# Kernel tuning notes

Hardware: AMD Instinct MI355X
Metric: run time of the kernel (lower is better)

## Reference

```python
import jax, jax.numpy as jnp
import numpy as np

NEG_INF = -1e30

def setup_inputs() -> dict:
    key = jax.random.key(0)
    kC, kQ, kw = jax.random.split(key, 3)
    B, D, Lc, Lq = 32, 128, 2048, 64
    C = jax.random.normal(kC, (B, D, Lc), dtype=jnp.float32)
    Q = jax.random.normal(kQ, (B, D, Lq), dtype=jnp.float32)
    qmask = jnp.ones((B, Lq), dtype=jnp.float32)
    # trilinear weight, uniform(-sqrt(1/D), sqrt(1/D)) as in the torch init
    lim = (1.0 / D) ** 0.5
    w = jax.random.uniform(kw, (3 * D,), dtype=jnp.float32, minval=-lim, maxval=lim)
    return {"C": C, "Q": Q, "qmask": qmask, "w": w}

def reference(C, Q, qmask, w):
    # C: (B, D, Lc), Q: (B, D, Lq), qmask: (B, Lq), w: (3D,)
    Ct = jnp.transpose(C, (0, 2, 1))  # (B, Lc, D)
    Qt = jnp.transpose(Q, (0, 2, 1))  # (B, Lq, D)
    D = Ct.shape[-1]
    w1, w2, w3 = w[:D], w[D:2 * D], w[2 * D:]
    # trilinear similarity S[b,i,j] = Ct[b,i].w1 + Qt[b,j].w2 + (Ct[b,i]*Qt[b,j]).w3
    # computed WITHOUT the (B,Lc,Lq,3D) intermediate
    sc = Ct @ w1                                   # (B, Lc)
    sq = Qt @ w2                                   # (B, Lq)
    scq = jnp.einsum('bid,bjd->bij', Ct * w3, Qt)  # (B, Lc, Lq)
    S = sc[:, :, None] + sq[None if False else slice(None), None, :] + scq  # (B, Lc, Lq)
    m = qmask[:, None, :]                          # (B, 1, Lq)
    S1 = jax.nn.softmax(S * m + (1.0 - m) * NEG_INF, axis=2)  # over query axis
    S2 = jax.nn.softmax(S, axis=1)                             # over context axis
    A = jnp.einsum('bij,bjd->bid', S1, Qt)                     # (B, Lc, D)
    S1S2T = jnp.einsum('bij,bkj->bik', S1, S2)                 # (B, Lc, Lc) via S1 @ S2^T
    Bm = jnp.einsum('bik,bkd->bid', S1S2T, Ct)                 # (B, Lc, D)
    out = jnp.concatenate([Ct, A, Ct * A, Ct * Bm], axis=2)    # (B, Lc, 4D)
    # dropout is identity in eval mode
    return jnp.transpose(out, (0, 2, 1))                       # (B, 4D, Lc)
```

## Files before the change

### kernel.cpp

```cpp
#include <hip/hip_runtime.h>

#define LC 2048
#define DD 128
#define LQ 64
#define NPART 16
#define PAD 136

typedef unsigned short u16;
typedef unsigned int u32;
typedef __attribute__((ext_vector_type(8))) short bf16x8;
typedef __attribute__((ext_vector_type(4))) float f32x4;

__device__ inline u16 f2b(float f) {
  u32 u = __float_as_uint(f);
  u32 r = (u + 0x7fffu + ((u >> 16) & 1u)) >> 16;
  return (u16)r;
}
__device__ inline float b2f(u16 u) { return __uint_as_float(((u32)u) << 16); }
__device__ inline u32 pack2(float a, float b) {
  return (u32)f2b(a) | ((u32)f2b(b) << 16);
}

__global__ __launch_bounds__(64) void k0_sq(const float* __restrict__ Q,
                                            const float* __restrict__ w,
                                            float* __restrict__ sqg) {
  int b = blockIdx.x, j = threadIdx.x;
  const float* Qb = Q + (size_t)b * DD * LQ + j;
  float acc = 0.f;
#pragma unroll 16
  for (int d = 0; d < DD; ++d) acc = fmaf(Qb[d * LQ], w[DD + d], acc);
  sqg[b * LQ + j] = acc;
}

__global__ __launch_bounds__(256) void k13(const float* __restrict__ C,
                                           const float* __restrict__ Q,
                                           const float* __restrict__ w,
                                           const float* __restrict__ sqg,
                                           u16* __restrict__ Eg,
                                           float* __restrict__ Tu_part,
                                           float* __restrict__ Z_part, int B) {
  __shared__ u16 ldsA[128 * PAD];
  __shared__ u16 ldsB[64 * PAD];
  __shared__ float scL[128];
  __shared__ float sqs[64];
  int b = blockIdx.y, bx = blockIdx.x;
  int i0 = bx * 128, t = threadIdx.x;
  const float* Cb = C + (size_t)b * DD * LC;
  const float* Qb = Q + (size_t)b * DD * LQ;
  if (t < 64) sqs[t] = sqg[b * LQ + t];
  int i_st = t & 127, dh = t >> 7;
  float scp = 0.f;
  {
    const float* Cp = Cb + (size_t)dh * 64 * LC + i0 + i_st;
#pragma unroll
    for (int dp = 0; dp < 32; ++dp) {
      int d = dh * 64 + 2 * dp;
      float c0 = Cp[(size_t)(2 * dp) * LC];
      float c1 = Cp[(size_t)(2 * dp + 1) * LC];
      scp = fmaf(c0, w[d], fmaf(c1, w[d + 1], scp));
      *(u32*)&ldsA[i_st * PAD + d] = pack2(c0, c1);
    }
    if (dh == 0) scL[i_st] = scp;
  }
  {
    int j = t & 63, dg = t >> 6;
    const float* Qp = Qb + j;
#pragma unroll
    for (int dp = 0; dp < 16; ++dp) {
      int d = dg * 32 + 2 * dp;
      float q0 = Qp[(size_t)d * LQ] * w[2 * DD + d];
      float q1 = Qp[(size_t)(d + 1) * LQ] * w[2 * DD + d + 1];
      *(u32*)&ldsB[j * PAD + d] = pack2(q0, q1);
    }
  }
  __syncthreads();
  if (dh == 1) scL[i_st] += scp;
  int lane = t & 63, wv = t >> 6;
  int lr = lane & 15, kg = lane >> 4;
  f32x4 acc[2][4];
#pragma unroll
  for (int mt = 0; mt < 2; ++mt)
#pragma unroll
    for (int nt = 0; nt < 4; ++nt) acc[mt][nt] = (f32x4){0.f, 0.f, 0.f, 0.f};
#pragma unroll
  for (int ks = 0; ks < 4; ++ks) {
    bf16x8 af[2], bf[4];
#pragma unroll
    for (int mt = 0; mt < 2; ++mt)
      af[mt] = *(bf16x8*)&ldsA[((wv * 2 + mt) * 16 + lr) * PAD + ks * 32 + kg * 8];
#pragma unroll
    for (int nt = 0; nt < 4; ++nt)
      bf[nt] = *(bf16x8*)&ldsB[(nt * 16 + lr) * PAD + ks * 32 + kg * 8];
#pragma unroll
    for (int mt = 0; mt < 2; ++mt)
#pragma unroll
      for (int nt = 0; nt < 4; ++nt)
        acc[mt][nt] = __builtin_amdgcn_mfma_f32_16x16x32_bf16(af[mt], bf[nt],
                                                              acc[mt][nt], 0, 0, 0);
  }
  __syncthreads();
#pragma unroll
  for (int mt = 0; mt < 2; ++mt) {
    int ib = (wv * 2 + mt) * 16 + kg * 4;
#pragma unroll
    for (int nt = 0; nt < 4; ++nt) {
      int j = nt * 16 + lr;
      float sqv = sqs[j];
      float e0 = __expf(acc[mt][nt][0] + scL[ib + 0] + sqv);
      float e1 = __expf(acc[mt][nt][1] + scL[ib + 1] + sqv);
      float e2 = __expf(acc[mt][nt][2] + scL[ib + 2] + sqv);
      float e3 = __expf(acc[mt][nt][3] + scL[ib + 3] + sqv);
      u32 pk[2] = {pack2(e0, e1), pack2(e2, e3)};
      *(uint2*)&ldsB[j * PAD + ib] = *(uint2*)pk;
    }
  }
  {
    int d = t >> 1, half = t & 1;
    const float* src = Cb + (size_t)d * LC + i0 + half * 64;
#pragma unroll
    for (int ip = 0; ip < 16; ++ip) {
      float4 v = *(const float4*)&src[ip * 4];
      u32 pk[2] = {pack2(v.x, v.y), pack2(v.z, v.w)};
      *(uint2*)&ldsA[d * PAD + half * 64 + ip * 4] = *(uint2*)pk;
    }
  }
  __syncthreads();
  if (t < 64) {
    const u32* row = (const u32*)&ldsB[t * PAD];
    float z = 0.f;
#pragma unroll
    for (int q = 0; q < 64; ++q) {
      u32 v = row[q];
      z += b2f((u16)v) + b2f((u16)(v >> 16));
    }
    Z_part[((size_t)bx * B + b) * LQ + t] = z;
  }
  {
    int i = t >> 1, half = t & 1;
    u32 opk[16];
#pragma unroll
    for (int q = 0; q < 16; ++q) {
      u16 a0 = ldsB[(half * 32 + 2 * q) * PAD + i];
      u16 a1 = ldsB[(half * 32 + 2 * q + 1) * PAD + i];
      opk[q] = (u32)a0 | ((u32)a1 << 16);
    }
    u16* dst = Eg + ((size_t)b * LC + i0 + i) * LQ + half * 32;
#pragma unroll
    for (int q = 0; q < 4; ++q) *(uint4*)&dst[q * 8] = *(uint4*)&opk[q * 4];
  }
  f32x4 tacc[2][4];
#pragma unroll
  for (int mt = 0; mt < 2; ++mt)
#pragma unroll
    for (int nt = 0; nt < 4; ++nt) tacc[mt][nt] = (f32x4){0.f, 0.f, 0.f, 0.f};
#pragma unroll
  for (int ks = 0; ks < 4; ++ks) {
    bf16x8 af[2], bf[4];
#pragma unroll
    for (int mt = 0; mt < 2; ++mt)
      af[mt] = *(bf16x8*)&ldsA[((wv * 2 + mt) * 16 + lr) * PAD + ks * 32 + kg * 8];
#pragma unroll
    for (int nt = 0; nt < 4; ++nt)
      bf[nt] = *(bf16x8*)&ldsB[(nt * 16 + lr) * PAD + ks * 32 + kg * 8];
#pragma unroll
    for (int mt = 0; mt < 2; ++mt)
#pragma unroll
      for (int nt = 0; nt < 4; ++nt)
        tacc[mt][nt] = __builtin_amdgcn_mfma_f32_16x16x32_bf16(af[mt], bf[nt],
                                                               tacc[mt][nt], 0, 0, 0);
  }
  float* Tp = Tu_part + ((size_t)bx * B + b) * LQ * DD;
#pragma unroll
  for (int mt = 0; mt < 2; ++mt)
#pragma unroll
    for (int nt = 0; nt < 4; ++nt) {
      int j = nt * 16 + lr;
      int db = (wv * 2 + mt) * 16 + kg * 4;
      *(f32x4*)&Tp[(size_t)j * DD + db] = tacc[mt][nt];
    }
}

__global__ __launch_bounds__(256) void k3b(const float* __restrict__ Tu_part,
                                           const float* __restrict__ Z_part,
                                           u16* __restrict__ TzT, int B) {
  __shared__ float Tsm[16][68];
  __shared__ float ziL[64];
  int b = blockIdx.y, d0 = blockIdx.x * 16;
  int t = threadIdx.x;
  int dd = t & 15, jg = t >> 4;
  float acc[4] = {};
#pragma unroll
  for (int p = 0; p < NPART; ++p) {
    const float* src = Tu_part + ((size_t)p * B + b) * LQ * DD + d0 + dd;
#pragma unroll
    for (int jj = 0; jj < 4; ++jj) acc[jj] += src[(jg * 4 + jj) * DD];
  }
  if (t < 64) {
    float z = 0.f;
#pragma unroll
    for (int p = 0; p < NPART; ++p) z += Z_part[((size_t)p * B + b) * LQ + t];
    ziL[t] = 1.f / z;
  }
  *(float4*)&Tsm[dd][jg * 4] = make_float4(acc[0], acc[1], acc[2], acc[3]);
  __syncthreads();
  if (t < 128) {
    int d = t >> 3, seg = t & 7;
    u32 pk[4];
#pragma unroll
    for (int q = 0; q < 4; ++q) {
      int j = seg * 8 + q * 2;
      pk[q] = pack2(Tsm[d][j] * ziL[j], Tsm[d][j + 1] * ziL[j + 1]);
    }
    *(uint4*)&TzT[((size_t)b * DD + d0 + d) * LQ + seg * 8] = *(uint4*)pk;
  }
}

__global__ __launch_bounds__(256) void k4(const u16* __restrict__ Eg,
                                          const float* __restrict__ qmask,
                                          const float* __restrict__ Q,
                                          const u16* __restrict__ TzT,
                                          const float* __restrict__ C,
                                          float* __restrict__ out) {
  __shared__ u16 S1L[128 * 72];
  __shared__ u16 QtL[128 * 72];
  __shared__ u16 TzL[128 * 72];
  __shared__ float mkL[64];
  int b = blockIdx.y, i0 = blockIdx.x * 128, t = threadIdx.x;
  if (t < 64) mkL[t] = qmask[b * LQ + t];
  __syncthreads();
  {
    int row = t >> 1, half = t & 1;
    const float* qsrc = Q + (size_t)b * DD * LQ + row * LQ + half * 32;
    u32 qpk[16];
#pragma unroll
    for (int q = 0; q < 16; ++q) qpk[q] = pack2(qsrc[2 * q], qsrc[2 * q + 1]);
#pragma unroll
    for (int q = 0; q < 4; ++q)
      *(uint4*)&QtL[row * 72 + half * 32 + q * 8] = *(uint4*)&qpk[q * 4];
    const u16* tsrc = TzT + ((size_t)b * DD + row) * LQ + half * 32;
#pragma unroll
    for (int q = 0; q < 4; ++q)
      *(uint4*)&TzL[row * 72 + half * 32 + q * 8] = *(const uint4*)&tsrc[q * 8];
    const u16* esrc = Eg + ((size_t)b * LC + i0 + row) * LQ + half * 32;
    u16 lv[32];
#pragma unroll
    for (int q = 0; q < 4; ++q)
      *(uint4*)&lv[q * 8] = *(const uint4*)&esrc[q * 8];
    float ev[32], ps = 0.f;
#pragma unroll
    for (int q = 0; q < 32; ++q) {
      ev[q] = b2f(lv[q]) * mkL[half * 32 + q];
      ps += ev[q];
    }
    ps += __shfl_xor(ps, 1);
    float inv = 1.f / fmaxf(ps, 1e-30f);
    u32 opk[16];
#pragma unroll
    for (int q = 0; q < 16; ++q)
      opk[q] = pack2(ev[2 * q] * inv, ev[2 * q + 1] * inv);
#pragma unroll
    for (int q = 0; q < 4; ++q)
      *(uint4*)&S1L[row * 72 + half * 32 + q * 8] = *(uint4*)&opk[q * 4];
  }
  __syncthreads();
  int lane = t & 63, wv = t >> 6;
  int lr = lane & 15, kg = lane >> 4;
  bf16x8 Bf[2][2];
#pragma unroll
  for (int it = 0; it < 2; ++it)
#pragma unroll
    for (int ks = 0; ks < 2; ++ks)
      Bf[it][ks] =
          *(bf16x8*)&S1L[(wv * 32 + it * 16 + lr) * 72 + ks * 32 + kg * 8];
  const float* Cb = C + (size_t)b * DD * LC + i0;
  float* outb = out + (size_t)b * 4 * DD * LC + i0;
#pragma unroll
  for (int dt = 0; dt < 8; ++dt) {
    bf16x8 QA[2], TA[2];
#pragma unroll
    for (int ks = 0; ks < 2; ++ks) {
      QA[ks] = *(bf16x8*)&QtL[(dt * 16 + lr) * 72 + ks * 32 + kg * 8];
      TA[ks] = *(bf16x8*)&TzL[(dt * 16 + lr) * 72 + ks * 32 + kg * 8];
    }
#pragma unroll
    for (int it = 0; it < 2; ++it) {
      f32x4 accA = {0.f, 0.f, 0.f, 0.f}, accB = {0.f, 0.f, 0.f, 0.f};
      accA = __builtin_amdgcn_mfma_f32_16x16x32_bf16(QA[0], Bf[it][0], accA, 0, 0, 0);
      accA = __builtin_amdgcn_mfma_f32_16x16x32_bf16(QA[1], Bf[it][1], accA, 0, 0, 0);
      accB = __builtin_amdgcn_mfma_f32_16x16x32_bf16(TA[0], Bf[it][0], accB, 0, 0, 0);
      accB = __builtin_amdgcn_mfma_f32_16x16x32_bf16(TA[1], Bf[it][1], accB, 0, 0, 0);
      int ii = wv * 32 + it * 16 + lr;
#pragma unroll
      for (int r = 0; r < 4; ++r) {
        int d = dt * 16 + kg * 4 + r;
        float c = Cb[(size_t)d * LC + ii];
        float a = accA[r], bm = accB[r];
        outb[(size_t)d * LC + ii] = c;
        outb[(size_t)(DD + d) * LC + ii] = a;
        outb[(size_t)(2 * DD + d) * LC + ii] = c * a;
        outb[(size_t)(3 * DD + d) * LC + ii] = c * bm;
      }
    }
  }
}

extern "C" void kernel_launch(void* const* d_in, const int* in_sizes, int n_in,
                              void* d_out, int out_size, void* d_ws, size_t ws_size,
                              hipStream_t stream) {
  const float* C = (const float*)d_in[0];
  const float* Q = (const float*)d_in[1];
  const float* qmask = (const float*)d_in[2];
  const float* w = (const float*)d_in[3];
  float* out = (float*)d_out;
  int B = in_sizes[2] / LQ;

  char* p = (char*)d_ws;
  u16* Eg = (u16*)p;            p += (size_t)B * LC * LQ * 2;
  u16* TzT = (u16*)p;           p += (size_t)B * DD * LQ * 2;
  float* Tu_part = (float*)p;   p += (size_t)NPART * B * LQ * DD * 4;
  float* Z_part = (float*)p;    p += (size_t)NPART * B * LQ * 4;
  float* sqg = (float*)p;

  k0_sq<<<B, 64, 0, stream>>>(Q, w, sqg);
  k13<<<dim3(NPART, B), 256, 0, stream>>>(C, Q, w, sqg, Eg, Tu_part, Z_part, B);
  k3b<<<dim3(DD / 16, B), 256, 0, stream>>>(Tu_part, Z_part, TzT, B);
  k4<<<dim3(LC / 128, B), 256, 0, stream>>>(Eg, qmask, Q, TzT, C, out);
}
```

Measured before the change: 76.91 us.

## Fuse sq and row-softmax normalization into k13, drop k0 and k4 LDS staging

Removes the separate k0_sq launch by computing the query-weight dot product inside k13 while Q is staged. The masked row softmax for S1 is finished in k13 using cross-lane shuffle reductions, so normalized S1 is written to global memory instead of raw exponentials. k4 then loads its MFMA operands straight from global memory (S1, Q converted to bf16 in registers, TzT) instead of staging them through shared memory, which removes its LDS buffers and barriers. In exchange, k13 does extra shuffle and normalization work, and k4 relies on uncoalesced global fragment loads that may be repeated across waves.

```diff
diff --git a/kernel.cpp b/kernel.cpp
--- a/kernel.cpp
+++ b/kernel.cpp
@@ -21,33 +21,23 @@
   return (u32)f2b(a) | ((u32)f2b(b) << 16);
 }
 
-__global__ __launch_bounds__(64) void k0_sq(const float* __restrict__ Q,
-                                            const float* __restrict__ w,
-                                            float* __restrict__ sqg) {
-  int b = blockIdx.x, j = threadIdx.x;
-  const float* Qb = Q + (size_t)b * DD * LQ + j;
-  float acc = 0.f;
-#pragma unroll 16
-  for (int d = 0; d < DD; ++d) acc = fmaf(Qb[d * LQ], w[DD + d], acc);
-  sqg[b * LQ + j] = acc;
-}
-
 __global__ __launch_bounds__(256) void k13(const float* __restrict__ C,
                                            const float* __restrict__ Q,
                                            const float* __restrict__ w,
-                                           const float* __restrict__ sqg,
-                                           u16* __restrict__ Eg,
+                                           const float* __restrict__ qmask,
+                                           u16* __restrict__ S1g,
                                            float* __restrict__ Tu_part,
                                            float* __restrict__ Z_part, int B) {
   __shared__ u16 ldsA[128 * PAD];
   __shared__ u16 ldsB[64 * PAD];
   __shared__ float scL[128];
   __shared__ float sqs[64];
+  __shared__ float mkS[64];
   int b = blockIdx.y, bx = blockIdx.x;
   int i0 = bx * 128, t = threadIdx.x;
   const float* Cb = C + (size_t)b * DD * LC;
   const float* Qb = Q + (size_t)b * DD * LQ;
-  if (t < 64) sqs[t] = sqg[b * LQ + t];
+  if (t < 64) mkS[t] = qmask[b * LQ + t];
   int i_st = t & 127, dh = t >> 7;
   float scp = 0.f;
   {
@@ -65,16 +55,23 @@
   {
     int j = t & 63, dg = t >> 6;
     const float* Qp = Qb + j;
+    float sqp = 0.f;
 #pragma unroll
     for (int dp = 0; dp < 16; ++dp) {
       int d = dg * 32 + 2 * dp;
-      float q0 = Qp[(size_t)d * LQ] * w[2 * DD + d];
-      float q1 = Qp[(size_t)(d + 1) * LQ] * w[2 * DD + d + 1];
-      *(u32*)&ldsB[j * PAD + d] = pack2(q0, q1);
-    }
+      float q0 = Qp[(size_t)d * LQ];
+      float q1 = Qp[(size_t)(d + 1) * LQ];
+      sqp = fmaf(q0, w[DD + d], fmaf(q1, w[DD + d + 1], sqp));
+      *(u32*)&ldsB[j * PAD + d] = pack2(q0 * w[2 * DD + d], q1 * w[2 * DD + d + 1]);
+    }
+    ((float*)&ldsB[j * PAD + 128])[dg] = sqp;
   }
   __syncthreads();
   if (dh == 1) scL[i_st] += scp;
+  if (t < 64) {
+    const float* pp = (const float*)&ldsB[t * PAD + 128];
+    sqs[t] = pp[0] + pp[1] + pp[2] + pp[3];
+  }
   int lane = t & 63, wv = t >> 6;
   int lr = lane & 15, kg = lane >> 4;
   f32x4 acc[2][4];
@@ -102,16 +99,39 @@
 #pragma unroll
   for (int mt = 0; mt < 2; ++mt) {
     int ib = (wv * 2 + mt) * 16 + kg * 4;
+    float ev[4][4];
+    float ps[4] = {0.f, 0.f, 0.f, 0.f};
 #pragma unroll
     for (int nt = 0; nt < 4; ++nt) {
       int j = nt * 16 + lr;
       float sqv = sqs[j];
-      float e0 = __expf(acc[mt][nt][0] + scL[ib + 0] + sqv);
-      float e1 = __expf(acc[mt][nt][1] + scL[ib + 1] + sqv);
-      float e2 = __expf(acc[mt][nt][2] + scL[ib + 2] + sqv);
-      float e3 = __expf(acc[mt][nt][3] + scL[ib + 3] + sqv);
-      u32 pk[2] = {pack2(e0, e1), pack2(e2, e3)};
+      float mkv = mkS[j];
+#pragma unroll
+      for (int r = 0; r < 4; ++r) {
+        float e = __expf(acc[mt][nt][r] + scL[ib + r] + sqv);
+        ev[nt][r] = e;
+        ps[r] = fmaf(mkv, e, ps[r]);
+      }
+    }
+#pragma unroll
+    for (int r = 0; r < 4; ++r) {
+      ps[r] += __shfl_xor(ps[r], 1, 64);
+      ps[r] += __shfl_xor(ps[r], 2, 64);
+      ps[r] += __shfl_xor(ps[r], 4, 64);
+      ps[r] += __shfl_xor(ps[r], 8, 64);
+    }
+#pragma unroll
+    for (int nt = 0; nt < 4; ++nt) {
+      int j = nt * 16 + lr;
+      u32 pk[2] = {pack2(ev[nt][0], ev[nt][1]), pack2(ev[nt][2], ev[nt][3])};
       *(uint2*)&ldsB[j * PAD + ib] = *(uint2*)pk;
+    }
+    if (lr == 0) {
+#pragma unroll
+      for (int r = 0; r < 4; ++r) {
+        int i = ib + r;
+        ((float*)&ldsB[(i & 63) * PAD + 128])[i >> 6] = 1.f / fmaxf(ps[r], 1e-30f);
+      }
     }
   }
   {
@@ -137,14 +157,16 @@
   }
   {
     int i = t >> 1, half = t & 1;
+    float inv = ((float*)&ldsB[(i & 63) * PAD + 128])[i >> 6];
     u32 opk[16];
 #pragma unroll
     for (int q = 0; q < 16; ++q) {
-      u16 a0 = ldsB[(half * 32 + 2 * q) * PAD + i];
-      u16 a1 = ldsB[(half * 32 + 2 * q + 1) * PAD + i];
-      opk[q] = (u32)a0 | ((u32)a1 << 16);
-    }
-    u16* dst = Eg + ((size_t)b * LC + i0 + i) * LQ + half * 32;
+      int j = half * 32 + 2 * q;
+      float a0 = b2f(ldsB[j * PAD + i]) * mkS[j] * inv;
+      float a1 = b2f(ldsB[(j + 1) * PAD + i]) * mkS[j + 1] * inv;
+      opk[q] = pack2(a0, a1);
+    }
+    u16* dst = S1g + ((size_t)b * LC + i0 + i) * LQ + half * 32;
 #pragma unroll
     for (int q = 0; q < 4; ++q) *(uint4*)&dst[q * 8] = *(uint4*)&opk[q * 4];
   }
@@ -215,72 +237,39 @@
   }
 }
 
-__global__ __launch_bounds__(256) void k4(const u16* __restrict__ Eg,
-                                          const float* __restrict__ qmask,
+__global__ __launch_bounds__(256) void k4(const u16* __restrict__ S1g,
                                           const float* __restrict__ Q,
                                           const u16* __restrict__ TzT,
                                           const float* __restrict__ C,
                                           float* __restrict__ out) {
-  __shared__ u16 S1L[128 * 72];
-  __shared__ u16 QtL[128 * 72];
-  __shared__ u16 TzL[128 * 72];
-  __shared__ float mkL[64];
   int b = blockIdx.y, i0 = blockIdx.x * 128, t = threadIdx.x;
-  if (t < 64) mkL[t] = qmask[b * LQ + t];
-  __syncthreads();
-  {
-    int row = t >> 1, half = t & 1;
-    const float* qsrc = Q + (size_t)b * DD * LQ + row * LQ + half * 32;
-    u32 qpk[16];
-#pragma unroll
-    for (int q = 0; q < 16; ++q) qpk[q] = pack2(qsrc[2 * q], qsrc[2 * q + 1]);
-#pragma unroll
-    for (int q = 0; q < 4; ++q)
-      *(uint4*)&QtL[row * 72 + half * 32 + q * 8] = *(uint4*)&qpk[q * 4];
-    const u16* tsrc = TzT + ((size_t)b * DD + row) * LQ + half * 32;
-#pragma unroll
-    for (int q = 0; q < 4; ++q)
-      *(uint4*)&TzL[row * 72 + half * 32 + q * 8] = *(const uint4*)&tsrc[q * 8];
-    const u16* esrc = Eg + ((size_t)b * LC + i0 + row) * LQ + half * 32;
-    u16 lv[32];
-#pragma unroll
-    for (int q = 0; q < 4; ++q)
-      *(uint4*)&lv[q * 8] = *(const uint4*)&esrc[q * 8];
-    float ev[32], ps = 0.f;
-#pragma unroll
-    for (int q = 0; q < 32; ++q) {
-      ev[q] = b2f(lv[q]) * mkL[half * 32 + q];
-      ps += ev[q];
-    }
-    ps += __shfl_xor(ps, 1);
-    float inv = 1.f / fmaxf(ps, 1e-30f);
-    u32 opk[16];
-#pragma unroll
-    for (int q = 0; q < 16; ++q)
-      opk[q] = pack2(ev[2 * q] * inv, ev[2 * q + 1] * inv);
-#pragma unroll
-    for (int q = 0; q < 4; ++q)
-      *(uint4*)&S1L[row * 72 + half * 32 + q * 8] = *(uint4*)&opk[q * 4];
-  }
-  __syncthreads();
   int lane = t & 63, wv = t >> 6;
   int lr = lane & 15, kg = lane >> 4;
   bf16x8 Bf[2][2];
 #pragma unroll
-  for (int it = 0; it < 2; ++it)
+  for (int it = 0; it < 2; ++it) {
+    size_t ri = (size_t)b * LC + i0 + wv * 32 + it * 16 + lr;
 #pragma unroll
     for (int ks = 0; ks < 2; ++ks)
-      Bf[it][ks] =
-          *(bf16x8*)&S1L[(wv * 32 + it * 16 + lr) * 72 + ks * 32 + kg * 8];
+      Bf[it][ks] = *(const bf16x8*)&S1g[ri * LQ + ks * 32 + kg * 8];
+  }
+  const float* Qb = Q + (size_t)b * DD * LQ;
+  const u16* Tzb = TzT + (size_t)b * DD * LQ;
   const float* Cb = C + (size_t)b * DD * LC + i0;
   float* outb = out + (size_t)b * 4 * DD * LC + i0;
 #pragma unroll
   for (int dt = 0; dt < 8; ++dt) {
+    int da = dt * 16 + lr;
     bf16x8 QA[2], TA[2];
 #pragma unroll
     for (int ks = 0; ks < 2; ++ks) {
-      QA[ks] = *(bf16x8*)&QtL[(dt * 16 + lr) * 72 + ks * 32 + kg * 8];
-      TA[ks] = *(bf16x8*)&TzL[(dt * 16 + lr) * 72 + ks * 32 + kg * 8];
+      const float* qp = Qb + da * LQ + ks * 32 + kg * 8;
+      float4 q0 = *(const float4*)qp;
+      float4 q1 = *(const float4*)(qp + 4);
+      u32 pk[4] = {pack2(q0.x, q0.y), pack2(q0.z, q0.w), pack2(q1.x, q1.y),
+                   pack2(q1.z, q1.w)};
+      QA[ks] = *(bf16x8*)pk;
+      TA[ks] = *(const bf16x8*)&Tzb[da * LQ + ks * 32 + kg * 8];
     }
 #pragma unroll
     for (int it = 0; it < 2; ++it) {
@@ -315,14 +304,12 @@
   int B = in_sizes[2] / LQ;
 
   char* p = (char*)d_ws;
-  u16* Eg = (u16*)p;            p += (size_t)B * LC * LQ * 2;
+  u16* S1g = (u16*)p;           p += (size_t)B * LC * LQ * 2;
   u16* TzT = (u16*)p;           p += (size_t)B * DD * LQ * 2;
   float* Tu_part = (float*)p;   p += (size_t)NPART * B * LQ * DD * 4;
-  float* Z_part = (float*)p;    p += (size_t)NPART * B * LQ * 4;
-  float* sqg = (float*)p;
-
-  k0_sq<<<B, 64, 0, stream>>>(Q, w, sqg);
-  k13<<<dim3(NPART, B), 256, 0, stream>>>(C, Q, w, sqg, Eg, Tu_part, Z_part, B);
+  float* Z_part = (float*)p;
+
+  k13<<<dim3(NPART, B), 256, 0, stream>>>(C, Q, w, qmask, S1g, Tu_part, Z_part, B);
   k3b<<<dim3(DD / 16, B), 256, 0, stream>>>(Tu_part, Z_part, TzT, B);
-  k4<<<dim3(LC / 128, B), 256, 0, stream>>>(Eg, qmask, Q, TzT, C, out);
-}
+  k4<<<dim3(LC / 128, B), 256, 0, stream>>>(S1g, Q, TzT, C, out);
+}
```

After: 71.58 us. 1.07x faster.
